# Performance work log

Measured on AMD Instinct MI355X. Metric: run time of the kernel, lower is better.

The kernel has to match this reference:

```python
import jax, jax.numpy as jnp
import numpy as np

D_MODEL = 128
NUM_HEADS = 8
DEPTH = D_MODEL // NUM_HEADS


def setup_inputs() -> dict:
    key = jax.random.key(0)
    ks = jax.random.split(key, 8)
    B, S = 4, 2048
    q = jax.random.normal(ks[0], (B, S, D_MODEL), dtype=jnp.float32)
    k = jax.random.normal(ks[1], (B, S, D_MODEL), dtype=jnp.float32)
    v = jax.random.normal(ks[2], (B, S, D_MODEL), dtype=jnp.float32)
    mask = (jax.random.uniform(ks[3], (B, 1, 1, S)) < 0.1).astype(jnp.float32)
    scale = 1.0 / np.sqrt(D_MODEL)
    wq_w = jax.random.normal(ks[4], (D_MODEL, D_MODEL), dtype=jnp.float32) * scale
    wq_b = jnp.zeros((D_MODEL,), dtype=jnp.float32)
    dense_w = jax.random.normal(ks[5], (D_MODEL, D_MODEL), dtype=jnp.float32) * scale
    dense_b = jnp.zeros((D_MODEL,), dtype=jnp.float32)
    return {"q": q, "k": k, "v": v, "mask": mask,
            "wq_w": wq_w, "wq_b": wq_b, "dense_w": dense_w, "dense_b": dense_b}


def _split_heads(x, B):
    # [B, S, d_model] -> [B, H, S, depth]
    return x.reshape(B, -1, NUM_HEADS, DEPTH).transpose(0, 2, 1, 3)


def reference(q, k, v, mask, wq_w, wq_b, dense_w, dense_b):
    B = q.shape[0]
    # NOTE: original code (faithfully) uses wq for q, k AND v
    qp = q @ wq_w + wq_b
    kp = k @ wq_w + wq_b
    vp = v @ wq_w + wq_b
    qh = _split_heads(qp, B)  # [B,H,Sq,dp]
    kh = _split_heads(kp, B)  # [B,H,Sk,dp]
    vh = _split_heads(vp, B)
    logits = jnp.einsum('bhqd,bhkd->bhqk', qh, kh) / jnp.sqrt(
        jnp.asarray(DEPTH, dtype=jnp.float32))
    logits = logits + mask * -1e9
    attn = jax.nn.softmax(logits, axis=-1)  # [B,H,Sq,Sk]
    ctx = jnp.einsum('bhqk,bhkd->bhqd', attn, vh)  # [B,H,Sq,dp]
    # NOTE: original reshapes [B,H,S,dp] -> [B,S,d_model] WITHOUT transposing
    # heads back (bug preserved for faithfulness)
    ctx = ctx.reshape(B, -1, D_MODEL)
    out = ctx @ dense_w + dense_b
    return out, attn
```

## Files before the change

kernel.cpp:

```cpp
#include <hip/hip_runtime.h>
#include <cstddef>
#include <cstdint>

#define DM   128
#define NH   8
#define DP   16
#define SEQ  2048
#define BB   4
#define CK   128
#define NCH  (SEQ / CK)

__device__ __forceinline__ float dot16(const float4 a[4], const float4 b[4]) {
  float s = 0.f;
#pragma unroll
  for (int i = 0; i < 4; ++i)
    s += a[i].x * b[i].x + a[i].y * b[i].y + a[i].z * b[i].z + a[i].w * b[i].w;
  return s;
}

__device__ __forceinline__ void gemm128_body(
    const float* __restrict__ X, const float* __restrict__ W,
    const float* __restrict__ bias, float* __restrict__ out,
    int row0, int headsplit)
{
  __shared__ float xs[64][DM];
  const int t = threadIdx.x;
  {
    const float4* Xv = (const float4*)(X + (size_t)row0 * DM);
    float4* xsv = (float4*)&xs[0][0];
#pragma unroll
    for (int i = 0; i < 8; ++i) xsv[t + i * 256] = Xv[t + i * 256];
  }
  __syncthreads();
  const int cg = t & 31;
  const int rg = t >> 5;
  float acc[8][4];
#pragma unroll
  for (int i = 0; i < 8; ++i)
#pragma unroll
    for (int j = 0; j < 4; ++j) acc[i][j] = 0.f;

  for (int k = 0; k < DM; k += 4) {
    float4 w0 = *(const float4*)(W + (size_t)(k + 0) * DM + cg * 4);
    float4 w1 = *(const float4*)(W + (size_t)(k + 1) * DM + cg * 4);
    float4 w2 = *(const float4*)(W + (size_t)(k + 2) * DM + cg * 4);
    float4 w3 = *(const float4*)(W + (size_t)(k + 3) * DM + cg * 4);
#pragma unroll
    for (int i = 0; i < 8; ++i) {
      float4 xv = *(const float4*)(&xs[rg * 8 + i][k]);
      acc[i][0] += xv.x * w0.x + xv.y * w1.x + xv.z * w2.x + xv.w * w3.x;
      acc[i][1] += xv.x * w0.y + xv.y * w1.y + xv.z * w2.y + xv.w * w3.y;
      acc[i][2] += xv.x * w0.z + xv.y * w1.z + xv.z * w2.z + xv.w * w3.z;
      acc[i][3] += xv.x * w0.w + xv.y * w1.w + xv.z * w2.w + xv.w * w3.w;
    }
  }
  float4 bv = *(const float4*)(bias + cg * 4);
#pragma unroll
  for (int i = 0; i < 8; ++i) {
    int row = row0 + rg * 8 + i;
    float4 o;
    o.x = acc[i][0] + bv.x; o.y = acc[i][1] + bv.y;
    o.z = acc[i][2] + bv.z; o.w = acc[i][3] + bv.w;
    if (headsplit) {
      int b = row >> 11, s = row & (SEQ - 1);
      int col = cg * 4;
      int h = col >> 4, d = col & 15;
      *(float4*)(out + (((size_t)(b * NH + h) * SEQ + s) * DP + d)) = o;
    } else {
      *(float4*)(out + (size_t)row * DM + cg * 4) = o;
    }
  }
}

__global__ __launch_bounds__(256) void proj_kernel(
    const float* __restrict__ q, const float* __restrict__ k,
    const float* __restrict__ v, const float* __restrict__ W,
    const float* __restrict__ bias, float* __restrict__ ws)
{
  const float* X = (blockIdx.y == 0) ? q : (blockIdx.y == 1) ? k : v;
  float* out = ws + (size_t)blockIdx.y * ((size_t)BB * SEQ * DM);
  gemm128_body(X, W, bias, out, blockIdx.x * 64, 1);
}

__global__ __launch_bounds__(256) void dense_kernel(
    const float* __restrict__ ctx, const float* __restrict__ W,
    const float* __restrict__ bias, float* __restrict__ out)
{
  gemm128_body(ctx, W, bias, out, blockIdx.x * 64, 0);
}

__global__ __launch_bounds__(256) void attn_kernel(
    const float* __restrict__ qh, const float* __restrict__ kh,
    const float* __restrict__ vh, const float* __restrict__ mask,
    float* __restrict__ attn, float* __restrict__ ctx)
{
  const int t = threadIdx.x;
  const int lane = t & 63;
  const int w = t >> 6;
  const int bh = blockIdx.x >> 8;
  const int qt = blockIdx.x & 255;
  const int b = bh >> 3;
  const int r0 = qt * 8 + w * 2;

  const float4* K4 = (const float4*)(kh + (size_t)bh * SEQ * DP);
  const float4* V4 = (const float4*)(vh + (size_t)bh * SEQ * DP);
  const float* mp = mask + (size_t)b * SEQ;

  float4 qa[4], qb[4];
  {
    const float4* Q4 = (const float4*)(qh + ((size_t)bh * SEQ + r0) * DP);
#pragma unroll
    for (int s = 0; s < 4; ++s) { qa[s] = Q4[s]; qb[s] = Q4[4 + s]; }
  }

  float p0[2 * NCH], p1[2 * NCH];

#pragma unroll
  for (int cc = 0; cc < NCH; ++cc) {
    const float4* Ka = K4 + ((size_t)(cc * CK + lane)) * 4;
    const float4* Kb = Ka + 64 * 4;
    float4 ka[4], kb[4];
#pragma unroll
    for (int s = 0; s < 4; ++s) { ka[s] = Ka[s]; kb[s] = Kb[s]; }
    float m0 = mp[cc * CK + lane] * -1e9f;
    float m1 = mp[cc * CK + 64 + lane] * -1e9f;
    p0[2 * cc]     = dot16(ka, qa) * 0.25f + m0;
    p0[2 * cc + 1] = dot16(kb, qa) * 0.25f + m1;
    p1[2 * cc]     = dot16(ka, qb) * 0.25f + m0;
    p1[2 * cc + 1] = dot16(kb, qb) * 0.25f + m1;
  }

  float mx0 = p0[0], mx1 = p1[0];
#pragma unroll
  for (int j = 1; j < 2 * NCH; ++j) { mx0 = fmaxf(mx0, p0[j]); mx1 = fmaxf(mx1, p1[j]); }
#pragma unroll
  for (int m = 1; m < 64; m <<= 1) {
    mx0 = fmaxf(mx0, __shfl_xor(mx0, m));
    mx1 = fmaxf(mx1, __shfl_xor(mx1, m));
  }
  float s0 = 0.f, s1 = 0.f;
#pragma unroll
  for (int j = 0; j < 2 * NCH; ++j) {
    p0[j] = __expf(p0[j] - mx0); s0 += p0[j];
    p1[j] = __expf(p1[j] - mx1); s1 += p1[j];
  }
#pragma unroll
  for (int m = 1; m < 64; m <<= 1) { s0 += __shfl_xor(s0, m); s1 += __shfl_xor(s1, m); }
  const float inv0 = 1.0f / s0, inv1 = 1.0f / s1;

  {
    float* a0 = attn + ((size_t)bh * SEQ + r0) * SEQ;
    float* a1 = a0 + SEQ;
#pragma unroll
    for (int cc = 0; cc < NCH; ++cc) {
      __builtin_nontemporal_store(p0[2 * cc] * inv0,     &a0[cc * CK + lane]);
      __builtin_nontemporal_store(p0[2 * cc + 1] * inv0, &a0[cc * CK + 64 + lane]);
      __builtin_nontemporal_store(p1[2 * cc] * inv1,     &a1[cc * CK + lane]);
      __builtin_nontemporal_store(p1[2 * cc + 1] * inv1, &a1[cc * CK + 64 + lane]);
    }
  }

  float4 acc0[4], acc1[4];
#pragma unroll
  for (int s = 0; s < 4; ++s) {
    acc0[s] = make_float4(0.f, 0.f, 0.f, 0.f);
    acc1[s] = make_float4(0.f, 0.f, 0.f, 0.f);
  }
#pragma unroll
  for (int cc = 0; cc < NCH; ++cc) {
    const float4* Va = V4 + ((size_t)(cc * CK + lane)) * 4;
    const float4* Vb = Va + 64 * 4;
    float pa0 = p0[2 * cc], pb0 = p0[2 * cc + 1];
    float pa1 = p1[2 * cc], pb1 = p1[2 * cc + 1];
#pragma unroll
    for (int s = 0; s < 4; ++s) {
      float4 va = Va[s];
      float4 vb = Vb[s];
      acc0[s].x += pa0 * va.x + pb0 * vb.x;
      acc0[s].y += pa0 * va.y + pb0 * vb.y;
      acc0[s].z += pa0 * va.z + pb0 * vb.z;
      acc0[s].w += pa0 * va.w + pb0 * vb.w;
      acc1[s].x += pa1 * va.x + pb1 * vb.x;
      acc1[s].y += pa1 * va.y + pb1 * vb.y;
      acc1[s].z += pa1 * va.z + pb1 * vb.z;
      acc1[s].w += pa1 * va.w + pb1 * vb.w;
    }
  }
#pragma unroll
  for (int s = 0; s < 4; ++s) {
    acc0[s].x *= inv0; acc0[s].y *= inv0; acc0[s].z *= inv0; acc0[s].w *= inv0;
    acc1[s].x *= inv1; acc1[s].y *= inv1; acc1[s].z *= inv1; acc1[s].w *= inv1;
  }
#pragma unroll
  for (int m = 1; m < 64; m <<= 1) {
#pragma unroll
    for (int s = 0; s < 4; ++s) {
      acc0[s].x += __shfl_xor(acc0[s].x, m);
      acc0[s].y += __shfl_xor(acc0[s].y, m);
      acc0[s].z += __shfl_xor(acc0[s].z, m);
      acc0[s].w += __shfl_xor(acc0[s].w, m);
      acc1[s].x += __shfl_xor(acc1[s].x, m);
      acc1[s].y += __shfl_xor(acc1[s].y, m);
      acc1[s].z += __shfl_xor(acc1[s].z, m);
      acc1[s].w += __shfl_xor(acc1[s].w, m);
    }
  }
  if (lane == 0) {
    float4* c4 = (float4*)(ctx + ((size_t)bh * SEQ + r0) * DP);
#pragma unroll
    for (int s = 0; s < 4; ++s) { c4[s] = acc0[s]; c4[4 + s] = acc1[s]; }
  }
}

extern "C" void kernel_launch(void* const* d_in, const int* in_sizes, int n_in,
                              void* d_out, int out_size, void* d_ws, size_t ws_size,
                              hipStream_t stream) {
  const float* q    = (const float*)d_in[0];
  const float* k    = (const float*)d_in[1];
  const float* v    = (const float*)d_in[2];
  const float* mask = (const float*)d_in[3];
  const float* wq_w = (const float*)d_in[4];
  const float* wq_b = (const float*)d_in[5];
  const float* dw   = (const float*)d_in[6];
  const float* db   = (const float*)d_in[7];

  float* ws  = (float*)d_ws;
  float* qh  = ws;
  float* kh  = ws + 1048576;
  float* vh  = ws + 2097152;
  float* ctx = ws + 3145728;

  float* out  = (float*)d_out;
  float* attn = out + (size_t)BB * SEQ * DM;

  proj_kernel<<<dim3(128, 3), 256, 0, stream>>>(q, k, v, wq_w, wq_b, ws);
  attn_kernel<<<dim3(8192), 256, 0, stream>>>(qh, kh, vh, mask, attn, ctx);
  dense_kernel<<<dim3(128), 256, 0, stream>>>(ctx, dw, db, out);
}
```

Measured before the change: 1.269 ms.

## Process one query row per wave with paired-key lanes and tighter launch bounds

The attention kernel now gives each wavefront a single query row instead of two, which halves the per-thread score array and accumulators so more waves fit per CU (launch bounds 256,4). Each lane now handles two adjacent keys, so the mask is read and the attention matrix written as 8-byte vector accesses instead of scalar ones, and K/V reads per lane are contiguous. The grid doubles to 16384 blocks. In exchange, every K and V element is loaded once per query row rather than shared across two rows, doubling K/V traffic from cache, and the shuffle reductions are repeated per row.

New measurement: 2.800 ms. +120.7%, slower.

```diff
diff --git a/kernel.cpp b/kernel.cpp
--- a/kernel.cpp
+++ b/kernel.cpp
@@ -9,6 +9,8 @@
 #define BB   4
 #define CK   128
 #define NCH  (SEQ / CK)
+
+typedef float f32x2 __attribute__((ext_vector_type(2)));
 
 __device__ __forceinline__ float dot16(const float4 a[4], const float4 b[4]) {
   float s = 0.f;
@@ -89,7 +91,7 @@
   gemm128_body(ctx, W, bias, out, blockIdx.x * 64, 0);
 }
 
-__global__ __launch_bounds__(256) void attn_kernel(
+__global__ __launch_bounds__(256, 4) void attn_kernel(
     const float* __restrict__ qh, const float* __restrict__ kh,
     const float* __restrict__ vh, const float* __restrict__ mask,
     float* __restrict__ attn, float* __restrict__ ctx)
@@ -97,118 +99,93 @@
   const int t = threadIdx.x;
   const int lane = t & 63;
   const int w = t >> 6;
-  const int bh = blockIdx.x >> 8;
-  const int qt = blockIdx.x & 255;
+  const int bh = blockIdx.x >> 9;
+  const int qb = blockIdx.x & 511;
   const int b = bh >> 3;
-  const int r0 = qt * 8 + w * 2;
+  const int r = qb * 4 + w;
 
   const float4* K4 = (const float4*)(kh + (size_t)bh * SEQ * DP);
   const float4* V4 = (const float4*)(vh + (size_t)bh * SEQ * DP);
   const float* mp = mask + (size_t)b * SEQ;
 
-  float4 qa[4], qb[4];
+  float4 q[4];
   {
-    const float4* Q4 = (const float4*)(qh + ((size_t)bh * SEQ + r0) * DP);
-#pragma unroll
-    for (int s = 0; s < 4; ++s) { qa[s] = Q4[s]; qb[s] = Q4[4 + s]; }
-  }
-
-  float p0[2 * NCH], p1[2 * NCH];
+    const float4* Q4 = (const float4*)(qh + ((size_t)bh * SEQ + r) * DP);
+#pragma unroll
+    for (int s = 0; s < 4; ++s) q[s] = Q4[s];
+  }
+
+  float p[2 * NCH];
 
 #pragma unroll
   for (int cc = 0; cc < NCH; ++cc) {
-    const float4* Ka = K4 + ((size_t)(cc * CK + lane)) * 4;
-    const float4* Kb = Ka + 64 * 4;
+    const float4* Ka = K4 + ((size_t)(cc * CK + 2 * lane)) * 4;
     float4 ka[4], kb[4];
 #pragma unroll
-    for (int s = 0; s < 4; ++s) { ka[s] = Ka[s]; kb[s] = Kb[s]; }
-    float m0 = mp[cc * CK + lane] * -1e9f;
-    float m1 = mp[cc * CK + 64 + lane] * -1e9f;
-    p0[2 * cc]     = dot16(ka, qa) * 0.25f + m0;
-    p0[2 * cc + 1] = dot16(kb, qa) * 0.25f + m1;
-    p1[2 * cc]     = dot16(ka, qb) * 0.25f + m0;
-    p1[2 * cc + 1] = dot16(kb, qb) * 0.25f + m1;
-  }
-
-  float mx0 = p0[0], mx1 = p1[0];
-#pragma unroll
-  for (int j = 1; j < 2 * NCH; ++j) { mx0 = fmaxf(mx0, p0[j]); mx1 = fmaxf(mx1, p1[j]); }
-#pragma unroll
-  for (int m = 1; m < 64; m <<= 1) {
-    mx0 = fmaxf(mx0, __shfl_xor(mx0, m));
-    mx1 = fmaxf(mx1, __shfl_xor(mx1, m));
-  }
-  float s0 = 0.f, s1 = 0.f;
-#pragma unroll
-  for (int j = 0; j < 2 * NCH; ++j) {
-    p0[j] = __expf(p0[j] - mx0); s0 += p0[j];
-    p1[j] = __expf(p1[j] - mx1); s1 += p1[j];
-  }
-#pragma unroll
-  for (int m = 1; m < 64; m <<= 1) { s0 += __shfl_xor(s0, m); s1 += __shfl_xor(s1, m); }
-  const float inv0 = 1.0f / s0, inv1 = 1.0f / s1;
+    for (int s = 0; s < 4; ++s) { ka[s] = Ka[s]; kb[s] = Ka[4 + s]; }
+    f32x2 mv = *(const f32x2*)(mp + cc * CK + 2 * lane);
+    p[2 * cc]     = dot16(ka, q) * 0.25f + mv.x * -1e9f;
+    p[2 * cc + 1] = dot16(kb, q) * 0.25f + mv.y * -1e9f;
+  }
+
+  float mx = p[0];
+#pragma unroll
+  for (int j = 1; j < 2 * NCH; ++j) mx = fmaxf(mx, p[j]);
+#pragma unroll
+  for (int m = 1; m < 64; m <<= 1) mx = fmaxf(mx, __shfl_xor(mx, m));
+  float sum = 0.f;
+#pragma unroll
+  for (int j = 0; j < 2 * NCH; ++j) { p[j] = __expf(p[j] - mx); sum += p[j]; }
+#pragma unroll
+  for (int m = 1; m < 64; m <<= 1) sum += __shfl_xor(sum, m);
+  const float inv = 1.0f / sum;
 
   {
-    float* a0 = attn + ((size_t)bh * SEQ + r0) * SEQ;
-    float* a1 = a0 + SEQ;
+    float* a0 = attn + ((size_t)bh * SEQ + r) * SEQ;
 #pragma unroll
     for (int cc = 0; cc < NCH; ++cc) {
-      __builtin_nontemporal_store(p0[2 * cc] * inv0,     &a0[cc * CK + lane]);
-      __builtin_nontemporal_store(p0[2 * cc + 1] * inv0, &a0[cc * CK + 64 + lane]);
-      __builtin_nontemporal_store(p1[2 * cc] * inv1,     &a1[cc * CK + lane]);
-      __builtin_nontemporal_store(p1[2 * cc + 1] * inv1, &a1[cc * CK + 64 + lane]);
-    }
-  }
-
-  float4 acc0[4], acc1[4];
-#pragma unroll
-  for (int s = 0; s < 4; ++s) {
-    acc0[s] = make_float4(0.f, 0.f, 0.f, 0.f);
-    acc1[s] = make_float4(0.f, 0.f, 0.f, 0.f);
-  }
+      f32x2 o;
+      o.x = p[2 * cc] * inv;
+      o.y = p[2 * cc + 1] * inv;
+      __builtin_nontemporal_store(o, (f32x2*)(a0 + cc * CK + 2 * lane));
+    }
+  }
+
+  float4 acc[4];
+#pragma unroll
+  for (int s = 0; s < 4; ++s) acc[s] = make_float4(0.f, 0.f, 0.f, 0.f);
 #pragma unroll
   for (int cc = 0; cc < NCH; ++cc) {
-    const float4* Va = V4 + ((size_t)(cc * CK + lane)) * 4;
-    const float4* Vb = Va + 64 * 4;
-    float pa0 = p0[2 * cc], pb0 = p0[2 * cc + 1];
-    float pa1 = p1[2 * cc], pb1 = p1[2 * cc + 1];
+    const float4* Va = V4 + ((size_t)(cc * CK + 2 * lane)) * 4;
+    float pa = p[2 * cc], pb = p[2 * cc + 1];
 #pragma unroll
     for (int s = 0; s < 4; ++s) {
       float4 va = Va[s];
-      float4 vb = Vb[s];
-      acc0[s].x += pa0 * va.x + pb0 * vb.x;
-      acc0[s].y += pa0 * va.y + pb0 * vb.y;
-      acc0[s].z += pa0 * va.z + pb0 * vb.z;
-      acc0[s].w += pa0 * va.w + pb0 * vb.w;
-      acc1[s].x += pa1 * va.x + pb1 * vb.x;
-      acc1[s].y += pa1 * va.y + pb1 * vb.y;
-      acc1[s].z += pa1 * va.z + pb1 * vb.z;
-      acc1[s].w += pa1 * va.w + pb1 * vb.w;
+      float4 vb = Va[4 + s];
+      acc[s].x += pa * va.x + pb * vb.x;
+      acc[s].y += pa * va.y + pb * vb.y;
+      acc[s].z += pa * va.z + pb * vb.z;
+      acc[s].w += pa * va.w + pb * vb.w;
     }
   }
 #pragma unroll
   for (int s = 0; s < 4; ++s) {
-    acc0[s].x *= inv0; acc0[s].y *= inv0; acc0[s].z *= inv0; acc0[s].w *= inv0;
-    acc1[s].x *= inv1; acc1[s].y *= inv1; acc1[s].z *= inv1; acc1[s].w *= inv1;
+    acc[s].x *= inv; acc[s].y *= inv; acc[s].z *= inv; acc[s].w *= inv;
   }
 #pragma unroll
   for (int m = 1; m < 64; m <<= 1) {
 #pragma unroll
     for (int s = 0; s < 4; ++s) {
-      acc0[s].x += __shfl_xor(acc0[s].x, m);
-      acc0[s].y += __shfl_xor(acc0[s].y, m);
-      acc0[s].z += __shfl_xor(acc0[s].z, m);
-      acc0[s].w += __shfl_xor(acc0[s].w, m);
-      acc1[s].x += __shfl_xor(acc1[s].x, m);
-      acc1[s].y += __shfl_xor(acc1[s].y, m);
-      acc1[s].z += __shfl_xor(acc1[s].z, m);
-      acc1[s].w += __shfl_xor(acc1[s].w, m);
+      acc[s].x += __shfl_xor(acc[s].x, m);
+      acc[s].y += __shfl_xor(acc[s].y, m);
+      acc[s].z += __shfl_xor(acc[s].z, m);
+      acc[s].w += __shfl_xor(acc[s].w, m);
     }
   }
   if (lane == 0) {
-    float4* c4 = (float4*)(ctx + ((size_t)bh * SEQ + r0) * DP);
-#pragma unroll
-    for (int s = 0; s < 4; ++s) { c4[s] = acc0[s]; c4[4 + s] = acc1[s]; }
+    float4* c4 = (float4*)(ctx + ((size_t)bh * SEQ + r) * DP);
+#pragma unroll
+    for (int s = 0; s < 4; ++s) c4[s] = acc[s];
   }
 }
 
@@ -234,6 +211,6 @@
   float* attn = out + (size_t)BB * SEQ * DM;
 
   proj_kernel<<<dim3(128, 3), 256, 0, stream>>>(q, k, v, wq_w, wq_b, ws);
-  attn_kernel<<<dim3(8192), 256, 0, stream>>>(qh, kh, vh, mask, attn, ctx);
+  attn_kernel<<<dim3(16384), 256, 0, stream>>>(qh, kh, vh, mask, attn, ctx);
   dense_kernel<<<dim3(128), 256, 0, stream>>>(ctx, dw, db, out);
 }
```
